# Kernel optimization log

Measured on AMD Instinct MI355X. Metric: run time of the kernel, lower is better.

## Reference

```python
import jax, jax.numpy as jnp
import numpy as np

BATCH, SEQ = 4, 2048
D_MODEL, INNER, STATE, K, FFN = 384, 768, 16, 4, 1024


def setup_inputs() -> dict:
    key = jax.random.key(0)
    ks = jax.random.split(key, 12)
    def g(k, shape, scale=0.02):
        return jax.random.normal(k, shape, jnp.float32) * scale
    return {
        "x": jax.random.normal(ks[0], (BATCH, SEQ, D_MODEL), jnp.float32),
        "rms1_w": jnp.ones((D_MODEL,), jnp.float32),
        "rms2_w": jnp.ones((D_MODEL,), jnp.float32),
        "in_proj_w": g(ks[1], (D_MODEL, 2 * INNER)),
        "conv_w": g(ks[2], (K, INNER, INNER)),
        "conv_b": jnp.zeros((INNER,), jnp.float32),
        "x_proj_w": g(ks[3], (INNER, 2 * STATE)),
        "dt_proj_w": g(ks[4], (INNER, INNER)),
        "dt_proj_b": jnp.zeros((INNER,), jnp.float32),
        "A_log": jnp.log(jax.random.uniform(ks[5], (INNER, STATE), jnp.float32, 1.0, 16.0)),
        "D_param": jnp.ones((INNER,), jnp.float32),
        "out_proj_w": g(ks[6], (INNER, D_MODEL)),
        "ln_gamma": jnp.ones((D_MODEL,), jnp.float32),
        "ln_beta": jnp.zeros((D_MODEL,), jnp.float32),
        "gate_w": g(ks[7], (D_MODEL, FFN)),
        "up_w": g(ks[8], (D_MODEL, FFN)),
        "down_w": g(ks[9], (FFN, D_MODEL)),
    }


def rms_norm(x, w, eps=1e-6):
    norm = jnp.sqrt(jnp.mean(jnp.square(x), axis=-1, keepdims=True) + eps)
    return x / norm * w


def layer_norm(x, gamma, beta, eps=1e-5):
    mu = jnp.mean(x, axis=-1, keepdims=True)
    var = jnp.mean(jnp.square(x - mu), axis=-1, keepdims=True)
    return (x - mu) / jnp.sqrt(var + eps) * gamma + beta


def selective_scan(x, delta, A_log, Bm, Cm, Dp):
    # x, delta: [B,L,Di]; Bm, Cm: [B,L,N]; A_log: [Di,N]; Dp: [Di]
    delta = jax.nn.softplus(delta)
    A = -jnp.exp(A_log)                          # [Di,N]
    A_disc = jnp.exp(delta[..., None] * A)       # [B,L,Di,N]
    B_disc = delta[..., None] * Bm[:, :, None, :]  # [B,L,Di,N]
    xs = jnp.moveaxis(x, 1, 0)       # [L,B,Di]
    As = jnp.moveaxis(A_disc, 1, 0)  # [L,B,Di,N]
    Bs = jnp.moveaxis(B_disc, 1, 0)  # [L,B,Di,N]
    Cs = jnp.moveaxis(Cm, 1, 0)      # [L,B,N]
    h0 = jnp.zeros((x.shape[0], A_log.shape[0], A_log.shape[1]), x.dtype)
    def step(h, inp):
        x_t, A_t, B_t, C_t = inp
        h = A_t * h + B_t * x_t[..., None]          # [B,Di,N]
        y_t = jnp.einsum('bdn,bn->bd', h, C_t)      # [B,Di]
        return h, y_t
    _, ys = jax.lax.scan(step, h0, (xs, As, Bs, Cs))
    y = jnp.moveaxis(ys, 0, 1)       # [B,L,Di]
    return y + Dp * x


def mamba_core(h, in_proj_w, conv_w, conv_b, x_proj_w, dt_proj_w, dt_proj_b,
               A_log, D_param, out_proj_w, ln_gamma, ln_beta):
    xz = h @ in_proj_w                             # [B,L,2*Di]
    x_inner, z = jnp.split(xz, 2, axis=-1)
    # Conv1D SAME padding (k=4 -> pad (1,2)), channels-last, kernel [W,I,O]
    x_conv = jax.lax.conv_general_dilated(
        x_inner, conv_w, window_strides=(1,), padding='SAME',
        dimension_numbers=('NWC', 'WIO', 'NWC')) + conv_b
    x_conv = jax.nn.silu(x_conv)
    Bm, Cm = jnp.split(x_conv @ x_proj_w, 2, axis=-1)  # each [B,L,N]
    delta = x_conv @ dt_proj_w + dt_proj_b            # [B,L,Di]
    y = selective_scan(x_conv, delta, A_log, Bm, Cm, D_param)
    y = y * jax.nn.silu(z)
    out = y @ out_proj_w
    return layer_norm(out, ln_gamma, ln_beta)


def reference(x, rms1_w, rms2_w, in_proj_w, conv_w, conv_b, x_proj_w,
              dt_proj_w, dt_proj_b, A_log, D_param, out_proj_w, ln_gamma,
              ln_beta, gate_w, up_w, down_w):
    residual = x
    h = rms_norm(x, rms1_w)
    h = mamba_core(h, in_proj_w, conv_w, conv_b, x_proj_w, dt_proj_w,
                   dt_proj_b, A_log, D_param, out_proj_w, ln_gamma, ln_beta)
    x = residual + h  # dropout inactive (training=False)
    residual = x
    h = rms_norm(x, rms2_w)
    hidden = jax.nn.silu(h @ gate_w) * (h @ up_w)
    x = residual + hidden @ down_w
    return x
```

## Files before the change

### kernel.cpp

```cpp
#include <hip/hip_runtime.h>
#include <hip/hip_bf16.h>


using u16 = unsigned short;
using u32 = unsigned int;
using short8 = __attribute__((ext_vector_type(8))) short;
using f32x4  = __attribute__((ext_vector_type(4))) float;

#define TTOK 8192
#define DM 384
#define DI 768
#define NST 16
#define LSEQ 2048
#define NCH 64
#define LCH 32

#define SWZ_R(row, quad) \
  ((row) * 32 + ((((quad) ^ (row) ^ ((row) >> 2)) & 3) * 8))
#define SWZ_W(tid) SWZ_R((tid) >> 2, (tid) & 3)

__device__ __forceinline__ float bf2f(u16 a) {
  u32 u = ((u32)a) << 16;
  float f; __builtin_memcpy(&f, &u, 4); return f;
}
__device__ __forceinline__ u16 f2bf(float f) {
  u32 u; __builtin_memcpy(&u, &f, 4);
  u32 r = (u + 0x7fffu + ((u >> 16) & 1u)) >> 16;
  return (u16)r;
}
__device__ __forceinline__ int probe_bf(const void* rw) {
  return (((const u32*)rw)[0] == 0x3F803F80u) ? 1 : 0;
}
__device__ __forceinline__ float ld_in(const void* p, int i, int isbf) {
  return isbf ? bf2f(((const u16*)p)[i]) : ((const float*)p)[i];
}
__device__ __forceinline__ float fexp2(float x) {
#if __has_builtin(__builtin_amdgcn_exp2f)
  return __builtin_amdgcn_exp2f(x);
#else
  return exp2f(x);
#endif
}
__device__ __forceinline__ float wave_sum(float v) {
#pragma unroll
  for (int off = 32; off > 0; off >>= 1) v += __shfl_xor(v, off, 64);
  return v;
}

__device__ __forceinline__ void gl_lds16(const u16* g, u16* l) {
  __builtin_amdgcn_global_load_lds(
      (const __attribute__((address_space(1))) u32*)g,
      (__attribute__((address_space(3))) u32*)l, 16, 0, 0);
}

#define V_CB 0
#define V_DB 768
#define V_DP 1536
#define V_R1 2304
#define V_R2 2688
#define V_GA 3072
#define V_BE 3456

__global__ __launch_bounds__(256) void k_prep(
    const void* __restrict__ x, const void* __restrict__ in_proj,
    const void* __restrict__ conv_w, const void* __restrict__ dt_w,
    const void* __restrict__ x_proj, const void* __restrict__ out_proj,
    const void* __restrict__ gate_w, const void* __restrict__ up_w,
    const void* __restrict__ down_w, const void* __restrict__ A_log,
    const void* __restrict__ conv_b, const void* __restrict__ dt_b,
    const void* __restrict__ Dp, const void* __restrict__ rms1_w,
    const void* __restrict__ rms2_w, const void* __restrict__ gamma,
    const void* __restrict__ beta,
    u16* __restrict__ W1T, u16* __restrict__ WCT, u16* __restrict__ W45T,
    u16* __restrict__ W5T, u16* __restrict__ W6T, u16* __restrict__ W7T,
    float* __restrict__ An2T, u16* __restrict__ vecs,
    u16* __restrict__ WinX, u16* __restrict__ h1pad) {
  const int isbf = probe_bf(rms1_w);
  const int bx = blockIdx.x;
  const int tid = threadIdx.x;
  __shared__ u16 lt[64 * 66];

  if (bx < 1236) {
    const void* src; size_t soff = 0; u16* dst; int R, C, tpr, lo;
    if (bx < 144)       { src = in_proj;  dst = W1T;  R = 384;  C = 1536; tpr = 24; lo = bx; }
    else if (bx < 720)  { int tp = (bx - 144) / 144; lo = (bx - 144) % 144;
                          src = conv_w; soff = (size_t)tp * 589824;
                          dst = WCT + (size_t)tp * 589824; R = 768; C = 768; tpr = 12; }
    else if (bx < 864)  { src = dt_w;     dst = W45T; R = 768;  C = 768;  tpr = 12; lo = bx - 720; }
    else if (bx < 876)  { src = x_proj;   dst = W45T + (size_t)768 * 768;
                          R = 768; C = 32; tpr = 1; lo = bx - 864; }
    else if (bx < 948)  { src = out_proj; dst = W5T;  R = 768;  C = 384;  tpr = 6;  lo = bx - 876; }
    else if (bx < 1044) { src = gate_w;   dst = W6T;  R = 384;  C = 1024; tpr = 16; lo = bx - 948; }
    else if (bx < 1140) { src = up_w;     dst = W6T + (size_t)1024 * 384;
                          R = 384; C = 1024; tpr = 16; lo = bx - 1044; }
    else                { src = down_w;   dst = W7T;  R = 1024; C = 384;  tpr = 6;  lo = bx - 1140; }
    int tr = lo / tpr, tc = lo % tpr;
    int r0 = tr * 64, c0 = tc * 64;
#pragma unroll
    for (int i = 0; i < 16; ++i) {
      int el = i * 256 + tid, lr = el >> 6, lc = el & 63;
      if (c0 + lc < C)
        lt[lr * 66 + lc] =
            f2bf(ld_in(src, (int)(soff + (size_t)(r0 + lr) * C + c0 + lc), isbf));
    }
    __syncthreads();
#pragma unroll
    for (int i = 0; i < 16; ++i) {
      int el = i * 256 + tid, orow = el >> 6, oc = el & 63;
      if (c0 + orow < C)
        dst[(size_t)(c0 + orow) * R + r0 + oc] = lt[oc * 66 + orow];
    }
    return;
  }
  if (bx < 5332) {
    int half = tid >> 7;
    int t = (bx - 1236) * 2 + half;
    int tid2 = tid & 127;
    int lane = tid & 63, wv = tid >> 6;
    float v[3]; float q = 0.f;
#pragma unroll
    for (int j = 0; j < 3; ++j) {
      v[j] = ld_in(x, t * DM + tid2 + j * 128, isbf);
      q += v[j] * v[j];
    }
    q = wave_sum(q);
    float* rq = (float*)lt;
    if (lane == 0) rq[wv] = q;
    __syncthreads();
    float rr = rsqrtf((rq[half * 2] + rq[half * 2 + 1]) * (1.f / DM) + 1e-6f);
    int b = t >> 11, l = t & 2047;
    size_t orow = ((size_t)(b * 2051 + l + 1)) * DM;
#pragma unroll
    for (int j = 0; j < 3; ++j) {
      int i = tid2 + j * 128;
      h1pad[orow + i] = f2bf(v[j] * rr * ld_in(rms1_w, i, isbf));
    }
    return;
  }
  if (bx < 6484) {
    int lo = (bx - 5332) * 256 + tid;
    int i = lo / 768, j = lo % 768;
    WinX[lo] = f2bf(ld_in(in_proj, i * 1536 + j, isbf));
    return;
  }
  if (bx < 6532) {
    int lo = (bx - 6484) * 256 + tid;
    if (lo < 12288) {
      int d = lo >> 4, n = lo & 15;
      An2T[n * DI + d] = -__expf(ld_in(A_log, lo, isbf)) * 1.44269504f;
    }
    return;
  }
  if (bx < 6547) {
    int lo = (bx - 6532) * 256 + tid;
    if (lo < 3840) {
      const void* s; int o;
      if      (lo < 768)  { s = conv_b; o = lo; }
      else if (lo < 1536) { s = dt_b;   o = lo - 768; }
      else if (lo < 2304) { s = Dp;     o = lo - 1536; }
      else if (lo < 2688) { s = rms1_w; o = lo - 2304; }
      else if (lo < 3072) { s = rms2_w; o = lo - 2688; }
      else if (lo < 3456) { s = gamma;  o = lo - 3072; }
      else                { s = beta;   o = lo - 3456; }
      vecs[lo] = f2bf(ld_in(s, o, isbf));
    }
    return;
  }
  {
    int lo = (bx - 6547) * 256 + tid;
    if (lo < 4608) {
      int b = lo / (3 * DM), rem = lo % (3 * DM);
      int which = rem / DM, i = rem % DM;
      int row = b * 2051 + (which == 0 ? 0 : (2048 + which));
      h1pad[(size_t)row * DM + i] = 0;
    }
  }
}

__global__ __launch_bounds__(128) void k_lnrms(const float* __restrict__ outm,
                                               const void* __restrict__ xin,
                                               const void* __restrict__ rw,
                                               const u16* __restrict__ vecs,
                                               float* __restrict__ x2f,
                                               u16* __restrict__ h2) {
  const int isbf = probe_bf(rw);
  int t = blockIdx.x, tid = threadIdx.x;
  int lane = tid & 63, wid = tid >> 6;
  float v[3]; float s = 0.f, q = 0.f;
#pragma unroll
  for (int j = 0; j < 3; ++j) {
    v[j] = outm[(size_t)t * DM + tid + j * 128];
    s += v[j]; q += v[j] * v[j];
  }
  s = wave_sum(s); q = wave_sum(q);
  __shared__ float rs[2], rq[2], r2[2];
  if (lane == 0) { rs[wid] = s; rq[wid] = q; }
  __syncthreads();
  float mu = (rs[0] + rs[1]) * (1.f / DM);
  float var = (rq[0] + rq[1]) * (1.f / DM) - mu * mu;
  float rstd = rsqrtf(var + 1e-5f);
  float x2v[3]; float q2 = 0.f;
#pragma unroll
  for (int j = 0; j < 3; ++j) {
    int i = tid + j * 128;
    float ln = (v[j] - mu) * rstd * bf2f(vecs[V_GA + i]) + bf2f(vecs[V_BE + i]);
    x2v[j] = ld_in(xin, t * DM + i, isbf) + ln;
    x2f[(size_t)t * DM + i] = x2v[j];
    q2 += x2v[j] * x2v[j];
  }
  q2 = wave_sum(q2);
  if (lane == 0) r2[wid] = q2;
  __syncthreads();
  float rr = rsqrtf((r2[0] + r2[1]) * (1.f / DM) + 1e-6f);
#pragma unroll
  for (int j = 0; j < 3; ++j) {
    int i = tid + j * 128;
    h2[(size_t)t * DM + i] = f2bf(x2v[j] * rr * bf2f(vecs[V_R2 + i]));
  }
}

template <int EPI, int KDIM>
__global__ __launch_bounds__(256) void gemm_bt(
    const u16* __restrict__ A, const u16* __restrict__ BT,
    float* __restrict__ o1, u16* __restrict__ ob1,
    const float* __restrict__ res, const void* __restrict__ fl) {
  __shared__ u16 smem[2][8192];
  const int tid = threadIdx.x;
  const int lane = tid & 63, wid = tid >> 6;
  const int wm = (wid >> 1) << 5, wn = (wid & 1) << 5;
  const int fr = lane & 15, quad = lane >> 4;
  const int m0 = blockIdx.x * 64, n0 = blockIdx.y * 64;

  f32x4 acc[2][2] = {};

  const int wrow = (wid << 4) | (lane >> 2);
  const int sq = ((lane & 3) ^ wrow ^ (wrow >> 2)) & 3;
  const u16* BTe = (EPI == 6) ? BT + (size_t)blockIdx.z * 589824 : BT;
  const u16* srcA = A + (size_t)(m0 + wrow) * KDIM + sq * 8;
  const u16* srcB = BTe + (size_t)(n0 + wrow) * KDIM + sq * 8;
  u16* lw = &smem[0][0] + (wid << 9);

  auto stage = [&](int buf, int kt) {
    u16* lb = lw + buf * 8192;
    gl_lds16(srcA + kt,      lb);
    gl_lds16(srcA + kt + 32, lb + 2048);
    gl_lds16(srcB + kt,      lb + 4096);
    gl_lds16(srcB + kt + 32, lb + 6144);
  };

  stage(0, 0);
  int cur = 0;

#pragma unroll 1
  for (int kt = 0; kt < KDIM; kt += 64) {
    __syncthreads();
    if (kt + 64 < KDIM) stage(cur ^ 1, kt + 64);
    const u16* sm = &smem[cur][0];
#pragma unroll
    for (int kh = 0; kh < 2; ++kh) {
      const int ao = kh * 2048, bo = 4096 + kh * 2048;
      short8 af[2], bfg[2];
#pragma unroll
      for (int i = 0; i < 2; ++i)
        af[i] = *(const short8*)&sm[ao + SWZ_R(wm + i * 16 + fr, quad)];
#pragma unroll
      for (int i = 0; i < 2; ++i)
        bfg[i] = *(const short8*)&sm[bo + SWZ_R(wn + i * 16 + fr, quad)];
#pragma unroll
      for (int mt = 0; mt < 2; ++mt)
#pragma unroll
        for (int nt = 0; nt < 2; ++nt)
          acc[mt][nt] = __builtin_amdgcn_mfma_f32_16x16x32_bf16(
              af[mt], bfg[nt], acc[mt][nt], 0, 0, 0);
    }
    cur ^= 1;
  }

  int isbf = 0;
  if (EPI == 5) isbf = probe_bf(fl);

#pragma unroll
  for (int mt = 0; mt < 2; ++mt) {
#pragma unroll
    for (int nt = 0; nt < 2; ++nt) {
#pragma unroll
      for (int r = 0; r < 4; ++r) {
        int t = m0 + wm + mt * 16 + quad * 4 + r;
        int n = n0 + wn + nt * 16 + fr;
        float v = acc[mt][nt][r];
        if (EPI == 3) {
          o1[(size_t)t * DM + n] = v;
        } else if (EPI == 5) {
          float val = v + res[(size_t)t * DM + n];
          if (isbf) ob1[(size_t)t * DM + n] = f2bf(val);
          else      o1[(size_t)t * DM + n] = val;
        } else if (EPI == 6) {
          ob1[(size_t)n * 1536 + blockIdx.z * 384 + t] = f2bf(v);
        }
      }
    }
  }
}

__global__ __launch_bounds__(256) void gemm2_128(
    const u16* __restrict__ A, const u16* __restrict__ BT,
    float* __restrict__ o2, u16* __restrict__ ob1,
    const u16* __restrict__ bias) {
  constexpr int KDIM = 768;
  __shared__ u16 smem[2][12288];
  const int tid = threadIdx.x;
  const int lane = tid & 63, wid = tid >> 6;
  const int wm = (wid >> 1) << 6, wn = (wid & 1) << 5;
  const int fr = lane & 15, quad = lane >> 4;
  const int m0 = blockIdx.x * 128, n0 = blockIdx.y * 64;

  f32x4 acc[4][2] = {};

  const int ra = (wid << 5) | (lane >> 2);
  const int sqa = ((lane & 3) ^ ra ^ (ra >> 2)) & 3;
  const int rb = (wid << 4) | (lane >> 2);
  const int sqb = ((lane & 3) ^ rb ^ (rb >> 2)) & 3;
  const u16* srcA = A + (size_t)(m0 + ra) * KDIM + sqa * 8;
  const u16* srcB = BT + (size_t)(n0 + rb) * KDIM + sqb * 8;
  u16* lA = &smem[0][0] + (wid << 10);
  u16* lB = &smem[0][8192] + (wid << 9);

  auto stage = [&](int buf, int kt) {
    u16* a = lA + buf * 12288;
    u16* bb = lB + buf * 12288;
    gl_lds16(srcA + kt,                           a);
    gl_lds16(srcA + kt + (size_t)16 * KDIM,       a + 512);
    gl_lds16(srcA + kt + 32,                      a + 4096);
    gl_lds16(srcA + kt + 32 + (size_t)16 * KDIM,  a + 4608);
    gl_lds16(srcB + kt,       bb);
    gl_lds16(srcB + kt + 32,  bb + 2048);
  };

  stage(0, 0);
  int cur = 0;

#pragma unroll 1
  for (int kt = 0; kt < KDIM; kt += 64) {
    __syncthreads();
    if (kt + 64 < KDIM) stage(cur ^ 1, kt + 64);
    const u16* sm = &smem[cur][0];
#pragma unroll
    for (int kh = 0; kh < 2; ++kh) {
      const int ao = kh * 4096, bo = 8192 + kh * 2048;
      short8 af[4], bfg[2];
#pragma unroll
      for (int i = 0; i < 4; ++i)
        af[i] = *(const short8*)&sm[ao + SWZ_R(wm + i * 16 + fr, quad)];
#pragma unroll
      for (int i = 0; i < 2; ++i)
        bfg[i] = *(const short8*)&sm[bo + SWZ_R(wn + i * 16 + fr, quad)];
#pragma unroll
      for (int mt = 0; mt < 4; ++mt)
#pragma unroll
        for (int nt = 0; nt < 2; ++nt)
          acc[mt][nt] = __builtin_amdgcn_mfma_f32_16x16x32_bf16(
              af[mt], bfg[nt], acc[mt][nt], 0, 0, 0);
    }
    cur ^= 1;
  }

#pragma unroll
  for (int nt = 0; nt < 2; ++nt) {
    const int n = n0 + wn + nt * 16 + fr;
    if (n < DI) {
      const float bv = bf2f(bias[n]);
#pragma unroll
      for (int mt = 0; mt < 4; ++mt) {
#pragma unroll
        for (int r = 0; r < 4; ++r) {
          int t = m0 + wm + mt * 16 + quad * 4 + r;
          float xx = acc[mt][nt][r] + bv;
          float e = fexp2(xx * 1.44269504f);
          float sp = (xx > 20.f) ? xx : 0.69314718056f * __log2f(1.f + e);
          ob1[(size_t)t * DI + n] = f2bf(sp);
        }
      }
    } else if (n < DI + 32) {
#pragma unroll
      for (int mt = 0; mt < 4; ++mt) {
#pragma unroll
        for (int r = 0; r < 4; ++r) {
          int t = m0 + wm + mt * 16 + quad * 4 + r;
          o2[(size_t)t * 32 + (n - DI)] = acc[mt][nt][r];
        }
      }
    }
  }
}

__global__ __launch_bounds__(256) void gemm_xz(
    const u16* __restrict__ A, const u16* __restrict__ WC,
    const u16* __restrict__ WZ, u16* __restrict__ xconv,
    u16* __restrict__ zbuf, const u16* __restrict__ bias) {
  __shared__ u16 smem[2][12288];
  const int tid = threadIdx.x;
  const int lane = tid & 63, wid = tid >> 6;
  const int wm = (wid >> 1) << 6, wn = (wid & 1) << 5;
  const int fr = lane & 15, quad = lane >> 4;
  const int yb = blockIdx.y;
  const bool isz = yb >= 12;
  const int kd = isz ? 384 : 1536;
  const u16* BT = isz ? WZ : WC;
  const int kldb = isz ? 384 : 1536;
  const int n0 = (isz ? yb - 12 : yb) * 64;
  const int m0 = blockIdx.x * 128;

  f32x4 acc[4][2] = {};

  const int ra = (wid << 5) | (lane >> 2);
  const int sqa = ((lane & 3) ^ ra ^ (ra >> 2)) & 3;
  const int rb = (wid << 4) | (lane >> 2);
  const int sqb = ((lane & 3) ^ rb ^ (rb >> 2)) & 3;
  const u16* srcB = BT + (size_t)(n0 + rb) * kldb + sqb * 8;
  const int b = m0 >> 11, l0 = m0 & 2047;
  const u16* srcA0 =
      A + (size_t)(b * 2051 + l0 + ra + (isz ? 1 : 0)) * DM + sqa * 8;
  u16* lA = &smem[0][0] + (wid << 10);
  u16* lB = &smem[0][8192] + (wid << 9);

  int wc = 0, ic = 0;
  auto stage = [&](int buf, int kt) {
    const u16* sa = srcA0 + (size_t)wc * DM + ic;
    u16* a = lA + buf * 12288;
    u16* bb = lB + buf * 12288;
    gl_lds16(sa,                         a);
    gl_lds16(sa + (size_t)16 * DM,       a + 512);
    gl_lds16(sa + 32,                    a + 4096);
    gl_lds16(sa + 32 + (size_t)16 * DM,  a + 4608);
    gl_lds16(srcB + kt,       bb);
    gl_lds16(srcB + kt + 32,  bb + 2048);
    ic += 64; if (ic == 384) { ic = 0; ++wc; }
  };

  stage(0, 0);
  int cur = 0;

#pragma unroll 1
  for (int kt = 0; kt < kd; kt += 64) {
    __syncthreads();
    if (kt + 64 < kd) stage(cur ^ 1, kt + 64);
    const u16* sm = &smem[cur][0];
#pragma unroll
    for (int kh = 0; kh < 2; ++kh) {
      const int ao = kh * 4096, bo = 8192 + kh * 2048;
      short8 af[4], bfg[2];
#pragma unroll
      for (int i = 0; i < 4; ++i)
        af[i] = *(const short8*)&sm[ao + SWZ_R(wm + i * 16 + fr, quad)];
#pragma unroll
      for (int i = 0; i < 2; ++i)
        bfg[i] = *(const short8*)&sm[bo + SWZ_R(wn + i * 16 + fr, quad)];
#pragma unroll
      for (int mt = 0; mt < 4; ++mt)
#pragma unroll
        for (int nt = 0; nt < 2; ++nt)
          acc[mt][nt] = __builtin_amdgcn_mfma_f32_16x16x32_bf16(
              af[mt], bfg[nt], acc[mt][nt], 0, 0, 0);
    }
    cur ^= 1;
  }

#pragma unroll
  for (int mt = 0; mt < 4; ++mt) {
#pragma unroll
    for (int nt = 0; nt < 2; ++nt) {
#pragma unroll
      for (int r = 0; r < 4; ++r) {
        int t = m0 + wm + mt * 16 + quad * 4 + r;
        int n = n0 + wn + nt * 16 + fr;
        float v = acc[mt][nt][r];
        if (isz) {
          zbuf[(size_t)t * DI + n] = f2bf(v);
        } else {
          float xx = v + bf2f(bias[n]);
          float sg = 1.f / (1.f + __expf(-xx));
          xconv[(size_t)t * DI + n] = f2bf(xx * sg);
        }
      }
    }
  }
}

__global__ __launch_bounds__(256) void gemm_gu(
    const u16* __restrict__ A, const u16* __restrict__ W6T,
    u16* __restrict__ hid) {
  __shared__ u16 smem[16384];
  const int tid = threadIdx.x;
  const int lane = tid & 63, wid = tid >> 6;
  const int wm = (wid >> 1) << 6, wn = (wid & 1) << 5;
  const int fr = lane & 15, quad = lane >> 4;
  const int m0 = blockIdx.x * 128, n0 = blockIdx.y * 64;

  f32x4 accg[4][2] = {}, accu[4][2] = {};

  const int ra = (wid << 5) | (lane >> 2);
  const int sqa = ((lane & 3) ^ ra ^ (ra >> 2)) & 3;
  const int rb = (wid << 4) | (lane >> 2);
  const int sqb = ((lane & 3) ^ rb ^ (rb >> 2)) & 3;
  const u16* srcA = A + (size_t)(m0 + ra) * DM + sqa * 8;
  const u16* srcG = W6T + (size_t)(n0 + rb) * DM + sqb * 8;
  const u16* srcU = W6T + (size_t)(1024 + n0 + rb) * DM + sqb * 8;
  u16* lA = &smem[0] + (wid << 10);
  u16* lG = &smem[8192] + (wid << 9);
  u16* lU = &smem[12288] + (wid << 9);

  auto stage = [&](int kt) {
    gl_lds16(srcA + kt,                        lA);
    gl_lds16(srcA + kt + (size_t)16 * DM,      lA + 512);
    gl_lds16(srcA + kt + 32,                   lA + 4096);
    gl_lds16(srcA + kt + 32 + (size_t)16 * DM, lA + 4608);
    gl_lds16(srcG + kt,       lG);
    gl_lds16(srcG + kt + 32,  lG + 2048);
    gl_lds16(srcU + kt,       lU);
    gl_lds16(srcU + kt + 32,  lU + 2048);
  };

#pragma unroll 1
  for (int kt = 0; kt < DM; kt += 64) {
    __syncthreads();
    stage(kt);
    __syncthreads();
#pragma unroll
    for (int kh = 0; kh < 2; ++kh) {
      const int ao = kh * 4096, go = 8192 + kh * 2048, uo = 12288 + kh * 2048;
      short8 af[4], bg[2], bu[2];
#pragma unroll
      for (int i = 0; i < 4; ++i)
        af[i] = *(const short8*)&smem[ao + SWZ_R(wm + i * 16 + fr, quad)];
#pragma unroll
      for (int i = 0; i < 2; ++i) {
        bg[i] = *(const short8*)&smem[go + SWZ_R(wn + i * 16 + fr, quad)];
        bu[i] = *(const short8*)&smem[uo + SWZ_R(wn + i * 16 + fr, quad)];
      }
#pragma unroll
      for (int mt = 0; mt < 4; ++mt)
#pragma unroll
        for (int nt = 0; nt < 2; ++nt) {
          accg[mt][nt] = __builtin_amdgcn_mfma_f32_16x16x32_bf16(
              af[mt], bg[nt], accg[mt][nt], 0, 0, 0);
          accu[mt][nt] = __builtin_amdgcn_mfma_f32_16x16x32_bf16(
              af[mt], bu[nt], accu[mt][nt], 0, 0, 0);
        }
    }
  }

#pragma unroll
  for (int mt = 0; mt < 4; ++mt) {
#pragma unroll
    for (int nt = 0; nt < 2; ++nt) {
#pragma unroll
      for (int r = 0; r < 4; ++r) {
        int t = m0 + wm + mt * 16 + quad * 4 + r;
        int n = n0 + wn + nt * 16 + fr;
        float g = accg[mt][nt][r];
        float u = accu[mt][nt][r];
        float sg = 1.f / (1.f + __expf(-g));
        hid[(size_t)t * 1024 + n] = f2bf(g * sg * u);
      }
    }
  }
}

__global__ __launch_bounds__(256) void k_scan1(
    const u16* __restrict__ deltab, const u16* __restrict__ xconv,
    const float* __restrict__ BC, const float* __restrict__ An2T,
    float* __restrict__ hlb, float* __restrict__ Sb) {
  __shared__ float bcs[LCH * 32];
  int gid = blockIdx.x * 256 + threadIdx.x;
  int d = gid % DI, bc = gid / DI, c = bc & (NCH - 1), b = bc >> 6;
  int row0 = b * LSEQ + c * LCH;
  ((float4*)bcs)[threadIdx.x] =
      ((const float4*)(BC + (size_t)row0 * 32))[threadIdx.x];
  float An[NST];
#pragma unroll
  for (int n = 0; n < NST; ++n) An[n] = An2T[n * DI + d];
  float h[NST];
#pragma unroll
  for (int n = 0; n < NST; ++n) h[n] = 0.f;
  float S = 0.f;
  float dt = bf2f(deltab[(size_t)row0 * DI + d]);
  float xv = bf2f(xconv[(size_t)row0 * DI + d]);
  __syncthreads();
  for (int s = 0; s < LCH; ++s) {
    float dtc = dt, xvc = xv;
    if (s + 1 < LCH) {
      int r2 = row0 + s + 1;
      dt = bf2f(deltab[(size_t)r2 * DI + d]);
      xv = bf2f(xconv[(size_t)r2 * DI + d]);
    }
    const float4* br = (const float4*)&bcs[s * 32];
    float4 q0 = br[0], q1 = br[1], q2 = br[2], q3 = br[3];
    float Bm[NST] = {q0.x, q0.y, q0.z, q0.w, q1.x, q1.y, q1.z, q1.w,
                     q2.x, q2.y, q2.z, q2.w, q3.x, q3.y, q3.z, q3.w};
    float dxv = dtc * xvc;
    S += dtc;
#pragma unroll
    for (int n = 0; n < NST; ++n) {
      float a = fexp2(dtc * An[n]);
      h[n] = fmaf(a, h[n], dxv * Bm[n]);
    }
  }
  float4* ph = (float4*)(hlb + (size_t)gid * NST);
#pragma unroll
  for (int i = 0; i < 4; ++i)
    ph[i] = make_float4(h[4*i], h[4*i+1], h[4*i+2], h[4*i+3]);
  Sb[gid] = S;
}

__global__ __launch_bounds__(256) void k_scan2(const float* __restrict__ hlb,
                                               const float* __restrict__ Sb,
                                               const float* __restrict__ An2T,
                                               float* __restrict__ hin) {
  int gid = blockIdx.x * 256 + threadIdx.x;
  int n = gid & 15, bd = gid >> 4;
  int d = bd % DI, b = bd / DI;
  float An = An2T[n * DI + d];
  size_t base = ((size_t)(b * NCH) * DI + d) * NST + n;
  size_t sbase = (size_t)(b * NCH) * DI + d;
  const size_t cstride = (size_t)DI * NST;
  float H = 0.f;
  for (int c = 0; c < NCH; ++c) {
    size_t idx = base + (size_t)c * cstride;
    float P = fexp2(An * Sb[sbase + (size_t)c * DI]);
    hin[idx] = H;
    H = hlb[idx] + P * H;
  }
}

__global__ __launch_bounds__(256) void k_scan3(
    const u16* __restrict__ deltab, const u16* __restrict__ xconv,
    const float* __restrict__ BC, const float* __restrict__ An2T,
    const float* __restrict__ hinb, const u16* __restrict__ zb,
    const u16* __restrict__ vecs, u16* __restrict__ ys) {
  __shared__ float bcs[LCH * 32];
  int gid = blockIdx.x * 256 + threadIdx.x;
  int d = gid % DI, bc = gid / DI, c = bc & (NCH - 1), b = bc >> 6;
  int row0 = b * LSEQ + c * LCH;
  ((float4*)bcs)[threadIdx.x] =
      ((const float4*)(BC + (size_t)row0 * 32))[threadIdx.x];
  float An[NST];
#pragma unroll
  for (int n = 0; n < NST; ++n) An[n] = An2T[n * DI + d];
  float h[NST];
  {
    const float4* hp = (const float4*)(hinb + (size_t)gid * NST);
#pragma unroll
    for (int i = 0; i < 4; ++i) {
      float4 t = hp[i];
      h[4*i] = t.x; h[4*i+1] = t.y; h[4*i+2] = t.z; h[4*i+3] = t.w;
    }
  }
  float Dd = bf2f(vecs[V_DP + d]);
  float dt = bf2f(deltab[(size_t)row0 * DI + d]);
  float xv = bf2f(xconv[(size_t)row0 * DI + d]);
  float zv = bf2f(zb[(size_t)row0 * DI + d]);
  __syncthreads();
  for (int s = 0; s < LCH; ++s) {
    int row = row0 + s;
    float dtc = dt, xvc = xv, zvc = zv;
    if (s + 1 < LCH) {
      int r2 = row + 1;
      dt = bf2f(deltab[(size_t)r2 * DI + d]);
      xv = bf2f(xconv[(size_t)r2 * DI + d]);
      zv = bf2f(zb[(size_t)r2 * DI + d]);
    }
    const float4* br = (const float4*)&bcs[s * 32];
    float4 q0 = br[0], q1 = br[1], q2 = br[2], q3 = br[3];
    float4 c0 = br[4], c1 = br[5], c2 = br[6], c3 = br[7];
    float Bm[NST] = {q0.x, q0.y, q0.z, q0.w, q1.x, q1.y, q1.z, q1.w,
                     q2.x, q2.y, q2.z, q2.w, q3.x, q3.y, q3.z, q3.w};
    float Cm[NST] = {c0.x, c0.y, c0.z, c0.w, c1.x, c1.y, c1.z, c1.w,
                     c2.x, c2.y, c2.z, c2.w, c3.x, c3.y, c3.z, c3.w};
    float dxv = dtc * xvc;
    float yp[4] = {0.f, 0.f, 0.f, 0.f};
#pragma unroll
    for (int n = 0; n < NST; ++n) {
      float a = fexp2(dtc * An[n]);
      h[n] = fmaf(a, h[n], dxv * Bm[n]);
      yp[n & 3] = fmaf(h[n], Cm[n], yp[n & 3]);
    }
    float y = (yp[0] + yp[1]) + (yp[2] + yp[3]);
    float sz = zvc / (1.f + __expf(-zvc));
    ys[(size_t)row * DI + d] = f2bf((y + Dd * xvc) * sz);
  }
}

extern "C" void kernel_launch(void* const* d_in, const int* in_sizes, int n_in,
                              void* d_out, int out_size, void* d_ws,
                              size_t ws_size, hipStream_t stream) {
  (void)in_sizes; (void)n_in; (void)out_size;
  const void* x        = d_in[0];
  const void* rms1_w   = d_in[1];
  const void* rms2_w   = d_in[2];
  const void* in_proj  = d_in[3];
  const void* conv_w   = d_in[4];
  const void* conv_b   = d_in[5];
  const void* x_proj   = d_in[6];
  const void* dt_w     = d_in[7];
  const void* dt_b     = d_in[8];
  const void* A_log    = d_in[9];
  const void* Dp       = d_in[10];
  const void* out_proj = d_in[11];
  const void* gamma    = d_in[12];
  const void* beta     = d_in[13];
  const void* gate_w   = d_in[14];
  const void* up_w     = d_in[15];
  const void* down_w   = d_in[16];

  char* ws = (char*)d_ws;
  size_t off = 0;
  auto alloc = [&](size_t bytes) -> void* {
    void* p = ws + off;
    off = (off + bytes + 255) & ~(size_t)255;
    return p;
  };
  u16*   W1T   = (u16*)alloc((size_t)1536 * 384 * 2);
  u16*   WCT   = (u16*)alloc((size_t)4 * 768 * 768 * 2);
  u16*   W45T  = (u16*)alloc((size_t)896 * 768 * 2);
  u16*   W5T   = (u16*)alloc((size_t)384 * 768 * 2);
  u16*   W6T   = (u16*)alloc((size_t)2048 * 384 * 2);
  u16*   W7T   = (u16*)alloc((size_t)384 * 1024 * 2);
  float* An2T  = (float*)alloc((size_t)16 * 768 * 4);
  u16*   vecs  = (u16*)alloc(3840 * 2);
  u16*   WinX  = (u16*)alloc((size_t)384 * 768 * 2);
  u16*   WcombT= (u16*)alloc((size_t)768 * 1536 * 2);
  u16*   h1pad = (u16*)alloc((size_t)4 * 2051 * 384 * 2);
  u16*   zbuf  = (u16*)alloc((size_t)8192 * 768 * 2);
  u16*   xconv = (u16*)alloc((size_t)8192 * 768 * 2);
  u16*   deltab= (u16*)alloc((size_t)8192 * 768 * 2);
  float* BCb   = (float*)alloc((size_t)8192 * 32 * 4);
  float* hl    = (float*)alloc((size_t)196608 * 16 * 4);
  float* Pb    = (float*)alloc((size_t)196608 * 16 * 4);
  float* hin   = (float*)alloc((size_t)196608 * 16 * 4);
  float* Sb    = (float*)alloc((size_t)196608 * 4);
  u16*   ys   = (u16*)hl;
  float* outm = Pb;
  float* x2f  = hin;
  u16*   h2   = h1pad;
  u16*   hid  = (u16*)hl;

  if (off > ws_size) return;

  k_prep<<<6565, 256, 0, stream>>>(
      x, in_proj, conv_w, dt_w, x_proj, out_proj, gate_w, up_w, down_w,
      A_log, conv_b, dt_b, Dp, rms1_w, rms2_w, gamma, beta,
      W1T, WCT, W45T, W5T, W6T, W7T, An2T, vecs, WinX, h1pad);

  gemm_bt<6, 768><<<dim3(6, 12, 4), 256, 0, stream>>>(
      WinX, WCT, nullptr, WcombT, nullptr, nullptr);

  gemm_xz<<<dim3(64, 24), 256, 0, stream>>>(
      h1pad, WcombT, W1T + (size_t)768 * 384, xconv, zbuf, vecs + V_CB);

  gemm2_128<<<dim3(64, 13), 256, 0, stream>>>(
      xconv, W45T, BCb, deltab, vecs + V_DB);

  k_scan1<<<768, 256, 0, stream>>>(deltab, xconv, BCb, An2T, hl, Sb);
  k_scan2<<<192, 256, 0, stream>>>(hl, Sb, An2T, hin);
  k_scan3<<<768, 256, 0, stream>>>(deltab, xconv, BCb, An2T, hin, zbuf, vecs,
                                   ys);

  gemm_bt<3, 768><<<dim3(128, 6), 256, 0, stream>>>(
      ys, W5T, outm, nullptr, nullptr, nullptr);
  k_lnrms<<<8192, 128, 0, stream>>>(outm, x, rms1_w, vecs, x2f, h2);

  gemm_gu<<<dim3(64, 16), 256, 0, stream>>>(h2, W6T, hid);
  gemm_bt<5, 1024><<<dim3(128, 6), 256, 0, stream>>>(
      hid, W7T, (float*)d_out, (u16*)d_out, x2f, rms1_w);
}
```

Measured before the change: 308.5 us.

## Move double buffering from xz GEMM to gate/up GEMM and prefetch scan2 loads

The xz GEMM drops its double-buffered LDS and goes back to single-buffer load/sync/compute, which halves its shared-memory footprint and may allow more resident blocks. The gate/up GEMM switches to a double-buffered pipeline with a 32-wide K step, so the next tile loads while the current one is computed. The chunk-carry scan kernel now loads the next chunk's hlb and Sb values one iteration ahead, hiding global-load latency in its serial loop. Together these shift where load/compute overlap is used. The costs are extra barriers in xz, and in gate/up twice as many iterations, each doing less work per barrier.

```diff
diff --git a/kernel.cpp b/kernel.cpp
--- a/kernel.cpp
+++ b/kernel.cpp
@@ -397,7 +397,7 @@
     const u16* __restrict__ A, const u16* __restrict__ WC,
     const u16* __restrict__ WZ, u16* __restrict__ xconv,
     u16* __restrict__ zbuf, const u16* __restrict__ bias) {
-  __shared__ u16 smem[2][12288];
+  __shared__ u16 smem[12288];
   const int tid = threadIdx.x;
   const int lane = tid & 63, wid = tid >> 6;
   const int wm = (wid >> 1) << 6, wn = (wid & 1) << 5;
@@ -420,41 +420,36 @@
   const int b = m0 >> 11, l0 = m0 & 2047;
   const u16* srcA0 =
       A + (size_t)(b * 2051 + l0 + ra + (isz ? 1 : 0)) * DM + sqa * 8;
-  u16* lA = &smem[0][0] + (wid << 10);
-  u16* lB = &smem[0][8192] + (wid << 9);
+  u16* lA = &smem[0] + (wid << 10);
+  u16* lB = &smem[8192] + (wid << 9);
 
   int wc = 0, ic = 0;
-  auto stage = [&](int buf, int kt) {
+  auto stage = [&](int kt) {
     const u16* sa = srcA0 + (size_t)wc * DM + ic;
-    u16* a = lA + buf * 12288;
-    u16* bb = lB + buf * 12288;
-    gl_lds16(sa,                         a);
-    gl_lds16(sa + (size_t)16 * DM,       a + 512);
-    gl_lds16(sa + 32,                    a + 4096);
-    gl_lds16(sa + 32 + (size_t)16 * DM,  a + 4608);
-    gl_lds16(srcB + kt,       bb);
-    gl_lds16(srcB + kt + 32,  bb + 2048);
+    gl_lds16(sa,                         lA);
+    gl_lds16(sa + (size_t)16 * DM,       lA + 512);
+    gl_lds16(sa + 32,                    lA + 4096);
+    gl_lds16(sa + 32 + (size_t)16 * DM,  lA + 4608);
+    gl_lds16(srcB + kt,       lB);
+    gl_lds16(srcB + kt + 32,  lB + 2048);
     ic += 64; if (ic == 384) { ic = 0; ++wc; }
   };
-
-  stage(0, 0);
-  int cur = 0;
 
 #pragma unroll 1
   for (int kt = 0; kt < kd; kt += 64) {
     __syncthreads();
-    if (kt + 64 < kd) stage(cur ^ 1, kt + 64);
-    const u16* sm = &smem[cur][0];
+    stage(kt);
+    __syncthreads();
 #pragma unroll
     for (int kh = 0; kh < 2; ++kh) {
       const int ao = kh * 4096, bo = 8192 + kh * 2048;
       short8 af[4], bfg[2];
 #pragma unroll
       for (int i = 0; i < 4; ++i)
-        af[i] = *(const short8*)&sm[ao + SWZ_R(wm + i * 16 + fr, quad)];
+        af[i] = *(const short8*)&smem[ao + SWZ_R(wm + i * 16 + fr, quad)];
 #pragma unroll
       for (int i = 0; i < 2; ++i)
-        bfg[i] = *(const short8*)&sm[bo + SWZ_R(wn + i * 16 + fr, quad)];
+        bfg[i] = *(const short8*)&smem[bo + SWZ_R(wn + i * 16 + fr, quad)];
 #pragma unroll
       for (int mt = 0; mt < 4; ++mt)
 #pragma unroll
@@ -462,7 +457,6 @@
           acc[mt][nt] = __builtin_amdgcn_mfma_f32_16x16x32_bf16(
               af[mt], bfg[nt], acc[mt][nt], 0, 0, 0);
     }
-    cur ^= 1;
   }
 
 #pragma unroll
@@ -489,7 +483,7 @@
 __global__ __launch_bounds__(256) void gemm_gu(
     const u16* __restrict__ A, const u16* __restrict__ W6T,
     u16* __restrict__ hid) {
-  __shared__ u16 smem[16384];
+  __shared__ u16 smem[2][8192];
   const int tid = threadIdx.x;
   const int lane = tid & 63, wid = tid >> 6;
   const int wm = (wid >> 1) << 6, wn = (wid & 1) << 5;
@@ -505,48 +499,47 @@
   const u16* srcA = A + (size_t)(m0 + ra) * DM + sqa * 8;
   const u16* srcG = W6T + (size_t)(n0 + rb) * DM + sqb * 8;
   const u16* srcU = W6T + (size_t)(1024 + n0 + rb) * DM + sqb * 8;
-  u16* lA = &smem[0] + (wid << 10);
-  u16* lG = &smem[8192] + (wid << 9);
-  u16* lU = &smem[12288] + (wid << 9);
-
-  auto stage = [&](int kt) {
-    gl_lds16(srcA + kt,                        lA);
-    gl_lds16(srcA + kt + (size_t)16 * DM,      lA + 512);
-    gl_lds16(srcA + kt + 32,                   lA + 4096);
-    gl_lds16(srcA + kt + 32 + (size_t)16 * DM, lA + 4608);
-    gl_lds16(srcG + kt,       lG);
-    gl_lds16(srcG + kt + 32,  lG + 2048);
-    gl_lds16(srcU + kt,       lU);
-    gl_lds16(srcU + kt + 32,  lU + 2048);
+  u16* lA = &smem[0][0] + (wid << 10);
+  u16* lG = &smem[0][4096] + (wid << 9);
+  u16* lU = &smem[0][6144] + (wid << 9);
+
+  auto stage = [&](int buf, int kt) {
+    u16* a = lA + buf * 8192;
+    u16* g = lG + buf * 8192;
+    u16* u = lU + buf * 8192;
+    gl_lds16(srcA + kt,                   a);
+    gl_lds16(srcA + kt + (size_t)16 * DM, a + 512);
+    gl_lds16(srcG + kt,                   g);
+    gl_lds16(srcU + kt,                   u);
   };
 
+  stage(0, 0);
+  int cur = 0;
+
 #pragma unroll 1
-  for (int kt = 0; kt < DM; kt += 64) {
+  for (int kt = 0; kt < DM; kt += 32) {
     __syncthreads();
-    stage(kt);
-    __syncthreads();
-#pragma unroll
-    for (int kh = 0; kh < 2; ++kh) {
-      const int ao = kh * 4096, go = 8192 + kh * 2048, uo = 12288 + kh * 2048;
-      short8 af[4], bg[2], bu[2];
-#pragma unroll
-      for (int i = 0; i < 4; ++i)
-        af[i] = *(const short8*)&smem[ao + SWZ_R(wm + i * 16 + fr, quad)];
-#pragma unroll
-      for (int i = 0; i < 2; ++i) {
-        bg[i] = *(const short8*)&smem[go + SWZ_R(wn + i * 16 + fr, quad)];
-        bu[i] = *(const short8*)&smem[uo + SWZ_R(wn + i * 16 + fr, quad)];
+    if (kt + 32 < DM) stage(cur ^ 1, kt + 32);
+    const u16* sm = &smem[cur][0];
+    short8 af[4], bg[2], bu[2];
+#pragma unroll
+    for (int i = 0; i < 4; ++i)
+      af[i] = *(const short8*)&sm[SWZ_R(wm + i * 16 + fr, quad)];
+#pragma unroll
+    for (int i = 0; i < 2; ++i) {
+      bg[i] = *(const short8*)&sm[4096 + SWZ_R(wn + i * 16 + fr, quad)];
+      bu[i] = *(const short8*)&sm[6144 + SWZ_R(wn + i * 16 + fr, quad)];
+    }
+#pragma unroll
+    for (int mt = 0; mt < 4; ++mt)
+#pragma unroll
+      for (int nt = 0; nt < 2; ++nt) {
+        accg[mt][nt] = __builtin_amdgcn_mfma_f32_16x16x32_bf16(
+            af[mt], bg[nt], accg[mt][nt], 0, 0, 0);
+        accu[mt][nt] = __builtin_amdgcn_mfma_f32_16x16x32_bf16(
+            af[mt], bu[nt], accu[mt][nt], 0, 0, 0);
       }
-#pragma unroll
-      for (int mt = 0; mt < 4; ++mt)
-#pragma unroll
-        for (int nt = 0; nt < 2; ++nt) {
-          accg[mt][nt] = __builtin_amdgcn_mfma_f32_16x16x32_bf16(
-              af[mt], bg[nt], accg[mt][nt], 0, 0, 0);
-          accu[mt][nt] = __builtin_amdgcn_mfma_f32_16x16x32_bf16(
-              af[mt], bu[nt], accu[mt][nt], 0, 0, 0);
-        }
-    }
+    cur ^= 1;
   }
 
 #pragma unroll
@@ -624,11 +617,17 @@
   size_t sbase = (size_t)(b * NCH) * DI + d;
   const size_t cstride = (size_t)DI * NST;
   float H = 0.f;
+  float hc = hlb[base], sc = Sb[sbase];
   for (int c = 0; c < NCH; ++c) {
     size_t idx = base + (size_t)c * cstride;
-    float P = fexp2(An * Sb[sbase + (size_t)c * DI]);
+    float hn = 0.f, sn = 0.f;
+    if (c + 1 < NCH) {
+      hn = hlb[idx + cstride];
+      sn = Sb[sbase + (size_t)(c + 1) * DI];
+    }
     hin[idx] = H;
-    H = hlb[idx] + P * H;
+    H = hc + fexp2(An * sc) * H;
+    hc = hn; sc = sn;
   }
 }
 
```

After: 298.8 us. 3.2% less time.
